# Optimization experiments

Measured on AMD Instinct MI355X. Metric: run time of the kernel, lower is better.

Reference implementation:

```python
import jax, jax.numpy as jnp
import numpy as np

B, S, D, H = 2, 4096, 512, 8
DK = D // H


def setup_inputs() -> dict:
    key = jax.random.key(0)
    ks = jax.random.split(key, 8)
    q = jax.random.normal(ks[0], (B, S, D), dtype=jnp.float32)
    k = jax.random.normal(ks[1], (B, S, D), dtype=jnp.float32)
    v = jax.random.normal(ks[2], (B, S, D), dtype=jnp.float32)
    mask = jax.random.randint(ks[3], (B, S, S), 0, 2, dtype=jnp.int32)
    scale = 1.0 / np.sqrt(D)
    w_q = jax.random.normal(ks[4], (D, D), dtype=jnp.float32) * scale
    w_k = jax.random.normal(ks[5], (D, D), dtype=jnp.float32) * scale
    w_v = jax.random.normal(ks[6], (D, D), dtype=jnp.float32) * scale
    w_o = jax.random.normal(ks[7], (D, D), dtype=jnp.float32) * scale
    return {"q": q, "k": k, "v": v, "mask": mask,
            "w_q": w_q, "w_k": w_k, "w_v": w_v, "w_o": w_o}


def reference(q, k, v, mask, w_q, w_k, w_v, w_o):
    # Projections (weights stored as [in, out]; no bias, matching bias=False)
    # [B,S,D] -> [B,H,S,DK]
    def split_heads(x):
        return x.reshape(B, S, H, DK).transpose(0, 2, 1, 3)

    qh = split_heads(q @ w_q)
    kh = split_heads(k @ w_k)
    vh = split_heads(v @ w_v)

    inv_sqrt_dk = jnp.float32(1.0 / np.sqrt(DK))
    # Explicit O(S^2) score matrix, as in the original module
    scores = jnp.einsum('bhqd,bhkd->bhqk', qh, kh) * inv_sqrt_dk
    scores = jnp.where(mask[:, None, :, :] == 0, jnp.float32(-1e9), scores)
    attn = jax.nn.softmax(scores, axis=-1)
    # dropout in eval mode (p=0) -> identity
    x = jnp.einsum('bhqk,bhkd->bhqd', attn, vh)
    x = x.transpose(0, 2, 1, 3).reshape(B, S, D)
    return x @ w_o
```

## Files before the change

### kernel.cpp

```cpp
#include <hip/hip_runtime.h>
#include <hip/hip_bf16.h>

#define Bn 2
#define Sn 4096
#define Dn 512
#define Hn 8
#define DKn 64

typedef __attribute__((ext_vector_type(8))) short bf16x8;
typedef __attribute__((ext_vector_type(4))) float f32x4;
typedef __attribute__((ext_vector_type(4))) _Float16 f16x4;
typedef __attribute__((ext_vector_type(8))) _Float16 f16x8;
typedef __attribute__((ext_vector_type(2))) _Float16 f16x2;
typedef __attribute__((ext_vector_type(8))) unsigned short us8;
typedef __attribute__((ext_vector_type(4))) unsigned short us4;

__device__ __forceinline__ unsigned short f2bf(float f) {
  unsigned u = __builtin_bit_cast(unsigned, f);
  u += 0x7fffu + ((u >> 16) & 1u);
  return (unsigned short)(u >> 16);
}

__global__ __launch_bounds__(256) void pack_mask_k(const int* __restrict__ mask,
                                                   unsigned int* __restrict__ pm) {
  int gid = blockIdx.x * 256 + threadIdx.x;
  int m = mask[gid];
  unsigned long long bal = __ballot(m != 0);
  if ((threadIdx.x & 63) == 0) {
    int q = (gid >> 12) & 4095;
    int b = gid >> 24;
    int kvw = (gid >> 5) & 127;
    pm[((size_t)b * 128 + kvw) * 4096 + q] = (unsigned)bal;
    pm[((size_t)b * 128 + kvw + 1) * 4096 + q] = (unsigned)(bal >> 32);
  }
}

__global__ __launch_bounds__(256) void cvt_k(const float* __restrict__ q,
                                             const float* __restrict__ k,
                                             const float* __restrict__ v,
                                             unsigned short* __restrict__ o) {
  const float* src = blockIdx.y == 0 ? q : blockIdx.y == 1 ? k : v;
  size_t i = (size_t)blockIdx.x * 256 + threadIdx.x;
  float4 f = *(const float4*)&src[i * 4];
  us4 r = {f2bf(f.x), f2bf(f.y), f2bf(f.z), f2bf(f.w)};
  *(us4*)&o[(size_t)blockIdx.y * (Bn * Sn * Dn) + i * 4] = r;
}

__global__ __launch_bounds__(256) void wt_k(const float* __restrict__ wq,
                                            const float* __restrict__ wk,
                                            const float* __restrict__ wv,
                                            const float* __restrict__ wo,
                                            unsigned short* __restrict__ wt) {
  __shared__ unsigned short ls[64][68];
  const float* W = blockIdx.z == 0 ? wq : blockIdx.z == 1 ? wk
                 : blockIdx.z == 2 ? wv : wo;
  int k0 = blockIdx.x * 64, n0 = blockIdx.y * 64;
  int t = threadIdx.x;
  for (int j = 0; j < 4; ++j) {
    int i = t + j * 256;
    int r = i >> 4, c4 = (i & 15) << 2;
    float4 f = *(const float4*)&W[(size_t)(k0 + r) * 512 + n0 + c4];
    ls[c4 + 0][r] = f2bf(f.x);
    ls[c4 + 1][r] = f2bf(f.y);
    ls[c4 + 2][r] = f2bf(f.z);
    ls[c4 + 3][r] = f2bf(f.w);
  }
  __syncthreads();
  unsigned short* out = wt + (size_t)blockIdx.z * 512 * 512;
  for (int j = 0; j < 4; ++j) {
    int i = t + j * 256;
    int r = i >> 4, c4 = (i & 15) << 2;
    us4 v = {ls[r][c4], ls[r][c4 + 1], ls[r][c4 + 2], ls[r][c4 + 3]};
    *(us4*)&out[(size_t)(n0 + r) * 512 + k0 + c4] = v;
  }
}

template <int MT, bool HEADS>
__global__ __launch_bounds__(256, 2) void gemm_k(
    const unsigned short* __restrict__ A0, size_t zstride,
    const unsigned short* __restrict__ wt, unsigned short* __restrict__ oh,
    unsigned short* __restrict__ vtg, float* __restrict__ olin) {
  __shared__ unsigned short smem[MT * 8192 + 16384];
  const int z = blockIdx.z;
  const unsigned short* A = A0 + zstride * z;
  const unsigned short* Wt = wt + (size_t)z * 512 * 512;
  const float scale = (HEADS && z == 0) ? 0.125f * 1.44269504088896f : 1.0f;
  const int m0 = blockIdx.x * (MT * 64), n0 = blockIdx.y * 128;
  const int t = threadIdx.x, w = t >> 6, l = t & 63;
  const int quad = l >> 4, c = l & 15;

  f32x4 acc[MT][8] = {};
  us8 apre[MT * 2], bpre[4];

#pragma unroll
  for (int j = 0; j < MT * 2; ++j) {
    int i = t + j * 256, r = i >> 3, u = i & 7;
    apre[j] = *(const us8*)&A[(size_t)(m0 + r) * 512 + (u << 3)];
  }
#pragma unroll
  for (int j = 0; j < 4; ++j) {
    int i = t + j * 256, r = i >> 3, u = i & 7;
    bpre[j] = *(const us8*)&Wt[(size_t)(n0 + r) * 512 + (u << 3)];
  }
#pragma unroll
  for (int j = 0; j < MT * 2; ++j) {
    int i = t + j * 256, r = i >> 3, u = i & 7;
    *(us8*)&smem[r * 64 + ((u ^ (r & 7)) << 3)] = apre[j];
  }
#pragma unroll
  for (int j = 0; j < 4; ++j) {
    int i = t + j * 256, r = i >> 3, u = i & 7;
    *(us8*)&smem[MT * 8192 + r * 64 + ((u ^ (r & 7)) << 3)] = bpre[j];
  }

  for (int k0 = 0; k0 < 512; k0 += 64) {
    const int cur = (k0 >> 6) & 1;
    const unsigned short* AsC = &smem[cur * (MT * 4096)];
    const unsigned short* BsC = &smem[MT * 8192 + cur * 8192];
    __syncthreads();
    const bool nxt = k0 + 64 < 512;
    if (nxt) {
#pragma unroll
      for (int j = 0; j < MT * 2; ++j) {
        int i = t + j * 256, r = i >> 3, u = i & 7;
        apre[j] = *(const us8*)&A[(size_t)(m0 + r) * 512 + k0 + 64 + (u << 3)];
      }
#pragma unroll
      for (int j = 0; j < 4; ++j) {
        int i = t + j * 256, r = i >> 3, u = i & 7;
        bpre[j] = *(const us8*)&Wt[(size_t)(n0 + r) * 512 + k0 + 64 + (u << 3)];
      }
    }

#pragma unroll
    for (int kc = 0; kc < 2; ++kc) {
      bf16x8 aA[MT], bB[8];
      int u = kc * 4 + quad;
#pragma unroll
      for (int mt = 0; mt < MT; ++mt) {
        int row = w * (MT * 16) + mt * 16 + c;
        aA[mt] = *(const bf16x8*)&AsC[row * 64 + ((u ^ (c & 7)) << 3)];
      }
#pragma unroll
      for (int nt = 0; nt < 8; ++nt) {
        int row = nt * 16 + c;
        bB[nt] = *(const bf16x8*)&BsC[row * 64 + ((u ^ (c & 7)) << 3)];
      }
#pragma unroll
      for (int mt = 0; mt < MT; ++mt)
#pragma unroll
        for (int nt = 0; nt < 8; ++nt)
          acc[mt][nt] = __builtin_amdgcn_mfma_f32_16x16x32_bf16(
              aA[mt], bB[nt], acc[mt][nt], 0, 0, 0);
    }

    if (nxt) {
      unsigned short* AsN = &smem[(cur ^ 1) * (MT * 4096)];
      unsigned short* BsN = &smem[MT * 8192 + (cur ^ 1) * 8192];
#pragma unroll
      for (int j = 0; j < MT * 2; ++j) {
        int i = t + j * 256, r = i >> 3, u = i & 7;
        *(us8*)&AsN[r * 64 + ((u ^ (r & 7)) << 3)] = apre[j];
      }
#pragma unroll
      for (int j = 0; j < 4; ++j) {
        int i = t + j * 256, r = i >> 3, u = i & 7;
        *(us8*)&BsN[r * 64 + ((u ^ (r & 7)) << 3)] = bpre[j];
      }
    }
  }

  if constexpr (HEADS) {
    if (z == 2) {
      __syncthreads();
#pragma unroll
      for (int mt = 0; mt < MT; ++mt) {
        int mb = w * (MT * 16) + mt * 16 + (quad << 2);
        int ml = (mb & 64) | (((mb >> 5) & 1) << 5) | (((mb >> 2) & 3) << 3) |
                 (((mb >> 4) & 1) << 2);
#pragma unroll
        for (int nt = 0; nt < 8; ++nt) {
          int nl = nt * 16 + c;
          us4 pk;
#pragma unroll
          for (int r = 0; r < 4; ++r)
            pk[r] = __builtin_bit_cast(unsigned short, (_Float16)acc[mt][nt][r]);
          *(us4*)&smem[nl * 152 + ml] = pk;
        }
      }
      __syncthreads();
      const int bb = m0 >> 12, sb = m0 & 4095;
#pragma unroll
      for (int j = 0; j < MT * 4; ++j) {
        int i = t + j * 256;
        int nl = i >> 4, mc = (i & 15) << 3;
        us8 vv = *(const us8*)&smem[nl * 152 + mc];
        int n = n0 + nl, hh = n >> 6, dk = n & 63;
        *(us8*)&vtg[((size_t)(bb * Hn + hh) * DKn + dk) * Sn + sb + mc] = vv;
      }
    } else {
#pragma unroll
      for (int mt = 0; mt < MT; ++mt)
#pragma unroll
        for (int nt = 0; nt < 8; ++nt)
#pragma unroll
          for (int r = 0; r < 4; ++r) {
            int m = m0 + w * (MT * 16) + mt * 16 + (quad << 2) + r;
            int n = n0 + nt * 16 + c;
            int b = m >> 12, s = m & 4095, hh = n >> 6, dk = n & 63;
            oh[(size_t)z * (Bn * Hn * Sn * DKn) +
               ((size_t)(b * Hn + hh) * Sn + s) * DKn + dk] =
                f2bf(acc[mt][nt][r] * scale);
          }
    }
  } else {
#pragma unroll
    for (int mt = 0; mt < MT; ++mt)
#pragma unroll
      for (int nt = 0; nt < 8; ++nt)
#pragma unroll
        for (int r = 0; r < 4; ++r) {
          int m = m0 + w * (MT * 16) + mt * 16 + (quad << 2) + r;
          int n = n0 + nt * 16 + c;
          olin[(size_t)m * 512 + n] = acc[mt][nt][r];
        }
  }
}

__global__ __launch_bounds__(512, 4) void flash_k(
    const unsigned short* __restrict__ Qh, const unsigned short* __restrict__ Kh,
    const unsigned short* __restrict__ VtG, const unsigned int* __restrict__ pmt,
    unsigned short* __restrict__ attn) {
  __shared__ unsigned short Ks[2][2][64 * 64];
  __shared__ unsigned short Vts[2][2][64 * 64];
  __shared__ unsigned int Mw[2][2][256];

  const int q0 = blockIdx.x * 128, h = blockIdx.y, b = blockIdx.z;
  const int t = threadIdx.x;
  const int g = t >> 8, tg = t & 255;
  const int w = (t >> 6) & 3, l = t & 63;
  const int quad = l >> 4, c = l & 15;
  const size_t hb = (size_t)(b * Hn + h) * Sn * DKn;
  const unsigned short* Qg = Qh + hb;
  const unsigned short* Kg = Kh + hb;
  const unsigned short* Vg = VtG + hb;

  bf16x8 bQ[2][2];
#pragma unroll
  for (int qf = 0; qf < 2; ++qf) {
    int qrow = q0 + w * 32 + qf * 16 + c;
#pragma unroll
    for (int kc = 0; kc < 2; ++kc)
      bQ[qf][kc] = *(const bf16x8*)&Qg[(size_t)qrow * 64 + kc * 32 + quad * 8];
  }

  f32x4 oacc[2][4] = {};
  float lsum[2] = {};
  const int sr = tg >> 3, su = tg & 7;
  const int off0 = sr * 64 + ((su ^ (sr & 7)) << 3);
  const int off1 = (sr + 32) * 64 + ((su ^ (sr & 7)) << 3);
  const f16x2 one2 = {(_Float16)1.0f, (_Float16)1.0f};

  us8 kpre[2], vpre[2];
  unsigned mpre;
  {
    const int kvF = g * 64;
    kpre[0] = *(const us8*)&Kg[(size_t)(kvF + sr) * 64 + (su << 3)];
    kpre[1] = *(const us8*)&Kg[(size_t)(kvF + sr + 32) * 64 + (su << 3)];
    vpre[0] = *(const us8*)&Vg[(size_t)sr * Sn + kvF + (su << 3)];
    vpre[1] = *(const us8*)&Vg[(size_t)(sr + 32) * Sn + kvF + (su << 3)];
    mpre = pmt[((size_t)b * 128 + (kvF >> 5) + (tg >> 7)) * 4096 + q0 + (tg & 127)];
    *(us8*)&Ks[g][0][off0] = kpre[0];
    *(us8*)&Ks[g][0][off1] = kpre[1];
    *(us8*)&Vts[g][0][off0] = vpre[0];
    *(us8*)&Vts[g][0][off1] = vpre[1];
    Mw[g][0][tg] = mpre;
  }

  for (int it = 0; it < 32; ++it) {
    const int cur = it & 1;
    __syncthreads();
    const bool nxt = it + 1 < 32;
    if (nxt) {
      const int kvN = (2 * (it + 1) + g) * 64;
      kpre[0] = *(const us8*)&Kg[(size_t)(kvN + sr) * 64 + (su << 3)];
      kpre[1] = *(const us8*)&Kg[(size_t)(kvN + sr + 32) * 64 + (su << 3)];
      vpre[0] = *(const us8*)&Vg[(size_t)sr * Sn + kvN + (su << 3)];
      vpre[1] = *(const us8*)&Vg[(size_t)(sr + 32) * Sn + kvN + (su << 3)];
      mpre = pmt[((size_t)b * 128 + (kvN >> 5) + (tg >> 7)) * 4096 + q0 + (tg & 127)];
    }

    f32x4 sacc[2][4] = {};
#pragma unroll
    for (int kc = 0; kc < 2; ++kc) {
      int u = kc * 4 + quad;
#pragma unroll
      for (int kvt = 0; kvt < 4; ++kvt) {
        int row = kvt * 16 + c;
        bf16x8 aK = *(const bf16x8*)&Ks[g][cur][row * 64 + ((u ^ (c & 7)) << 3)];
#pragma unroll
        for (int qf = 0; qf < 2; ++qf)
          sacc[qf][kvt] = __builtin_amdgcn_mfma_f32_16x16x32_bf16(
              aK, bQ[qf][kc], sacc[qf][kvt], 0, 0, 0);
      }
    }

    f16x8 ph[2][2];
#pragma unroll
    for (int qf = 0; qf < 2; ++qf) {
      int qloc = w * 32 + qf * 16 + c;
      unsigned mv0 = Mw[g][cur][qloc], mv1 = Mw[g][cur][128 + qloc];
#pragma unroll
      for (int half = 0; half < 2; ++half) {
        unsigned word = half ? mv1 : mv0;
        uint4 ww;
#pragma unroll
        for (int kvh = 0; kvh < 2; ++kvh) {
          unsigned bits = (word >> ((kvh << 4) + (quad << 2))) & 15u;
          const f32x4 s4 = sacc[qf][half * 2 + kvh];
          float p0 = (bits & 1u) ? __builtin_amdgcn_exp2f(s4[0]) : 0.f;
          float p1 = (bits & 2u) ? __builtin_amdgcn_exp2f(s4[1]) : 0.f;
          float p2 = (bits & 4u) ? __builtin_amdgcn_exp2f(s4[2]) : 0.f;
          float p3 = (bits & 8u) ? __builtin_amdgcn_exp2f(s4[3]) : 0.f;
          f16x2 a = __builtin_bit_cast(f16x2, __builtin_amdgcn_cvt_pkrtz(p0, p1));
          f16x2 bpk = __builtin_bit_cast(f16x2, __builtin_amdgcn_cvt_pkrtz(p2, p3));
          lsum[qf] = __builtin_amdgcn_fdot2(a, one2, lsum[qf], false);
          lsum[qf] = __builtin_amdgcn_fdot2(bpk, one2, lsum[qf], false);
          (&ww.x)[kvh * 2] = __builtin_bit_cast(unsigned, a);
          (&ww.x)[kvh * 2 + 1] = __builtin_bit_cast(unsigned, bpk);
        }
        ph[qf][half] = __builtin_bit_cast(f16x8, ww);
      }
    }

#pragma unroll
    for (int half = 0; half < 2; ++half) {
      int u2 = half * 4 + quad;
#pragma unroll
      for (int dkt = 0; dkt < 4; ++dkt) {
        int dk = dkt * 16 + c;
        f16x8 bV = __builtin_bit_cast(
            f16x8, *(const us8*)&Vts[g][cur][dk * 64 + ((u2 ^ (c & 7)) << 3)]);
#pragma unroll
        for (int qf = 0; qf < 2; ++qf)
          oacc[qf][dkt] = __builtin_amdgcn_mfma_f32_16x16x32_f16(
              ph[qf][half], bV, oacc[qf][dkt], 0, 0, 0);
      }
    }

    if (nxt) {
      const int nb = cur ^ 1;
      *(us8*)&Ks[g][nb][off0] = kpre[0];
      *(us8*)&Ks[g][nb][off1] = kpre[1];
      *(us8*)&Vts[g][nb][off0] = vpre[0];
      *(us8*)&Vts[g][nb][off1] = vpre[1];
      Mw[g][nb][tg] = mpre;
    }
  }

  __syncthreads();
  float* fsum = (float*)&Ks[0][0][0];
  float* flsum = (float*)&Vts[0][0][0];
  if (g == 1) {
#pragma unroll
    for (int qf = 0; qf < 2; ++qf) {
#pragma unroll
      for (int dkt = 0; dkt < 4; ++dkt)
        *(f32x4*)&fsum[(((qf * 4 + dkt) * 4 + w) * 64 + l) * 4] = oacc[qf][dkt];
      flsum[(qf * 4 + w) * 64 + l] = lsum[qf];
    }
  }
  __syncthreads();
  if (g == 0) {
#pragma unroll
    for (int qf = 0; qf < 2; ++qf) {
      lsum[qf] += flsum[(qf * 4 + w) * 64 + l];
#pragma unroll
      for (int dkt = 0; dkt < 4; ++dkt) {
        f32x4 o1 = *(const f32x4*)&fsum[(((qf * 4 + dkt) * 4 + w) * 64 + l) * 4];
#pragma unroll
        for (int r = 0; r < 4; ++r) oacc[qf][dkt][r] += o1[r];
      }
    }
#pragma unroll
    for (int qf = 0; qf < 2; ++qf) {
      float s = lsum[qf];
      s += __shfl_xor(s, 16, 64);
      s += __shfl_xor(s, 32, 64);
      float inv = 1.0f / s;
#pragma unroll
      for (int r = 0; r < 4; ++r) {
        float invr = __shfl(inv, (quad << 2) + r, 64);
        unsigned short* dst =
            &attn[((size_t)(b * Sn + q0 + w * 32 + qf * 16 + (quad << 2) + r)) * Dn +
                  h * 64 + c];
#pragma unroll
        for (int dkt = 0; dkt < 4; ++dkt)
          dst[dkt * 16] = f2bf(oacc[qf][dkt][r] * invr);
      }
    }
  }
}

extern "C" void kernel_launch(void* const* d_in, const int* in_sizes, int n_in,
                              void* d_out, int out_size, void* d_ws,
                              size_t ws_size, hipStream_t stream) {
  const float* q = (const float*)d_in[0];
  const float* k = (const float*)d_in[1];
  const float* v = (const float*)d_in[2];
  const int* mask = (const int*)d_in[3];
  const float* wq = (const float*)d_in[4];
  const float* wk = (const float*)d_in[5];
  const float* wv = (const float*)d_in[6];
  const float* wo = (const float*)d_in[7];
  float* out = (float*)d_out;

  char* ws = (char*)d_ws;
  const size_t headN = (size_t)Bn * Hn * Sn * DKn;
  const size_t tensB = headN * 2;
  unsigned short* qbkb = (unsigned short*)ws;
  unsigned short* attn = (unsigned short*)ws;
  size_t off = 3 * tensB;
  unsigned short* qkv = (unsigned short*)(ws + off);
  off += 3 * tensB;
  unsigned short* wt = (unsigned short*)(ws + off);
  off += 4ull * 512 * 512 * 2;
  unsigned int* pm = (unsigned int*)(ws + off);

  pack_mask_k<<<(Bn * Sn * Sn) / 256, 256, 0, stream>>>(mask, pm);
  cvt_k<<<dim3(4096, 3), 256, 0, stream>>>(q, k, v, qbkb);
  wt_k<<<dim3(8, 8, 4), 256, 0, stream>>>(wq, wk, wv, wo, wt);
  gemm_k<2, true><<<dim3(64, 4, 3), 256, 0, stream>>>(
      qbkb, headN, wt, qkv, qkv + 2 * headN, nullptr);
  flash_k<<<dim3(32, 8, 2), 512, 0, stream>>>(qkv, qkv + headN,
                                              qkv + 2 * headN, pm, attn);
  gemm_k<1, false><<<dim3(128, 4, 1), 256, 0, stream>>>(
      attn, 0, wt + 3ull * 512 * 512, nullptr, nullptr, out);
}
```

Baseline: 388.2 us.

## Fuse prep kernels, convert fp32 inputs inside GEMM, compute row sums via MFMA

The mask packing and weight transpose kernels are merged into one prep kernel, and the mask-packing blocks now loop over eight chunks each. The separate fp32-to-bf16 conversion of q/k/v is dropped; the projection GEMM reads fp32 directly and converts while loading tiles. This removes a full write and re-read of the converted activations plus two launches. In the flash kernel, the softmax row sums move from fdot2 accumulation onto an extra MFMA against a ones vector, which also removes the end-of-kernel shuffles. Pointer increments replace per-iteration address recomputation. In exchange, the GEMM pulls twice as many bytes from global memory per A tile, and each flash iteration issues more MFMAs.

```diff
diff --git a/kernel.cpp b/kernel.cpp
--- a/kernel.cpp
+++ b/kernel.cpp
@@ -21,68 +21,60 @@
   return (unsigned short)(u >> 16);
 }
 
-__global__ __launch_bounds__(256) void pack_mask_k(const int* __restrict__ mask,
-                                                   unsigned int* __restrict__ pm) {
-  int gid = blockIdx.x * 256 + threadIdx.x;
-  int m = mask[gid];
-  unsigned long long bal = __ballot(m != 0);
-  if ((threadIdx.x & 63) == 0) {
-    int q = (gid >> 12) & 4095;
-    int b = gid >> 24;
-    int kvw = (gid >> 5) & 127;
-    pm[((size_t)b * 128 + kvw) * 4096 + q] = (unsigned)bal;
-    pm[((size_t)b * 128 + kvw + 1) * 4096 + q] = (unsigned)(bal >> 32);
-  }
-}
-
-__global__ __launch_bounds__(256) void cvt_k(const float* __restrict__ q,
-                                             const float* __restrict__ k,
-                                             const float* __restrict__ v,
-                                             unsigned short* __restrict__ o) {
-  const float* src = blockIdx.y == 0 ? q : blockIdx.y == 1 ? k : v;
-  size_t i = (size_t)blockIdx.x * 256 + threadIdx.x;
-  float4 f = *(const float4*)&src[i * 4];
-  us4 r = {f2bf(f.x), f2bf(f.y), f2bf(f.z), f2bf(f.w)};
-  *(us4*)&o[(size_t)blockIdx.y * (Bn * Sn * Dn) + i * 4] = r;
-}
-
-__global__ __launch_bounds__(256) void wt_k(const float* __restrict__ wq,
-                                            const float* __restrict__ wk,
-                                            const float* __restrict__ wv,
-                                            const float* __restrict__ wo,
-                                            unsigned short* __restrict__ wt) {
-  __shared__ unsigned short ls[64][68];
-  const float* W = blockIdx.z == 0 ? wq : blockIdx.z == 1 ? wk
-                 : blockIdx.z == 2 ? wv : wo;
-  int k0 = blockIdx.x * 64, n0 = blockIdx.y * 64;
-  int t = threadIdx.x;
-  for (int j = 0; j < 4; ++j) {
-    int i = t + j * 256;
-    int r = i >> 4, c4 = (i & 15) << 2;
-    float4 f = *(const float4*)&W[(size_t)(k0 + r) * 512 + n0 + c4];
-    ls[c4 + 0][r] = f2bf(f.x);
-    ls[c4 + 1][r] = f2bf(f.y);
-    ls[c4 + 2][r] = f2bf(f.z);
-    ls[c4 + 3][r] = f2bf(f.w);
-  }
-  __syncthreads();
-  unsigned short* out = wt + (size_t)blockIdx.z * 512 * 512;
-  for (int j = 0; j < 4; ++j) {
-    int i = t + j * 256;
-    int r = i >> 4, c4 = (i & 15) << 2;
-    us4 v = {ls[r][c4], ls[r][c4 + 1], ls[r][c4 + 2], ls[r][c4 + 3]};
-    *(us4*)&out[(size_t)(n0 + r) * 512 + k0 + c4] = v;
+__global__ __launch_bounds__(256) void prep_k(
+    const int* __restrict__ mask, unsigned int* __restrict__ pm,
+    const float* __restrict__ wq, const float* __restrict__ wk,
+    const float* __restrict__ wv, const float* __restrict__ wo,
+    unsigned short* __restrict__ wt) {
+  const int t = threadIdx.x;
+  if (blockIdx.x < 256) {
+    __shared__ unsigned short ls[64][68];
+    int bid = blockIdx.x;
+    int z = bid >> 6, x = bid & 7, y = (bid >> 3) & 7;
+    const float* W = z == 0 ? wq : z == 1 ? wk : z == 2 ? wv : wo;
+    int k0 = x * 64, n0 = y * 64;
+    for (int j = 0; j < 4; ++j) {
+      int i = t + j * 256;
+      int r = i >> 4, c4 = (i & 15) << 2;
+      float4 f = *(const float4*)&W[(size_t)(k0 + r) * 512 + n0 + c4];
+      ls[c4 + 0][r] = f2bf(f.x);
+      ls[c4 + 1][r] = f2bf(f.y);
+      ls[c4 + 2][r] = f2bf(f.z);
+      ls[c4 + 3][r] = f2bf(f.w);
+    }
+    __syncthreads();
+    unsigned short* out = wt + (size_t)z * 512 * 512;
+    for (int j = 0; j < 4; ++j) {
+      int i = t + j * 256;
+      int r = i >> 4, c4 = (i & 15) << 2;
+      us4 v = {ls[r][c4], ls[r][c4 + 1], ls[r][c4 + 2], ls[r][c4 + 3]};
+      *(us4*)&out[(size_t)(n0 + r) * 512 + k0 + c4] = v;
+    }
+  } else {
+    size_t idx = (size_t)(blockIdx.x - 256) * 256 + t;
+    for (int it = 0; it < 8; ++it, idx += 4194304) {
+      int m = mask[idx];
+      unsigned long long bal = __ballot(m != 0);
+      if ((t & 63) == 0) {
+        int q = (int)((idx >> 12) & 4095);
+        int b = (int)(idx >> 24);
+        int kvw = (int)((idx >> 5) & 127);
+        pm[((size_t)b * 128 + kvw) * 4096 + q] = (unsigned)bal;
+        pm[((size_t)b * 128 + kvw + 1) * 4096 + q] = (unsigned)(bal >> 32);
+      }
+    }
   }
 }
 
 template <int MT, bool HEADS>
 __global__ __launch_bounds__(256, 2) void gemm_k(
-    const unsigned short* __restrict__ A0, size_t zstride,
+    const float* __restrict__ aq, const float* __restrict__ ak,
+    const float* __restrict__ av, const unsigned short* __restrict__ abf,
     const unsigned short* __restrict__ wt, unsigned short* __restrict__ oh,
     unsigned short* __restrict__ vtg, float* __restrict__ olin) {
   __shared__ unsigned short smem[MT * 8192 + 16384];
   const int z = blockIdx.z;
-  const unsigned short* A = A0 + zstride * z;
+  const float* A32 = HEADS ? (z == 0 ? aq : z == 1 ? ak : av) : nullptr;
   const unsigned short* Wt = wt + (size_t)z * 512 * 512;
   const float scale = (HEADS && z == 0) ? 0.125f * 1.44269504088896f : 1.0f;
   const int m0 = blockIdx.x * (MT * 64), n0 = blockIdx.y * 128;
@@ -92,11 +84,23 @@
   f32x4 acc[MT][8] = {};
   us8 apre[MT * 2], bpre[4];
 
-#pragma unroll
-  for (int j = 0; j < MT * 2; ++j) {
+  auto ldA = [&](int j, int kk) -> us8 {
     int i = t + j * 256, r = i >> 3, u = i & 7;
-    apre[j] = *(const us8*)&A[(size_t)(m0 + r) * 512 + (u << 3)];
-  }
+    if constexpr (HEADS) {
+      const float* s = &A32[(size_t)(m0 + r) * 512 + kk + (u << 3)];
+      float4 f0 = *(const float4*)s;
+      float4 f1 = *(const float4*)(s + 4);
+      us8 v;
+      v[0] = f2bf(f0.x); v[1] = f2bf(f0.y); v[2] = f2bf(f0.z); v[3] = f2bf(f0.w);
+      v[4] = f2bf(f1.x); v[5] = f2bf(f1.y); v[6] = f2bf(f1.z); v[7] = f2bf(f1.w);
+      return v;
+    } else {
+      return *(const us8*)&abf[(size_t)(m0 + r) * 512 + kk + (u << 3)];
+    }
+  };
+
+#pragma unroll
+  for (int j = 0; j < MT * 2; ++j) apre[j] = ldA(j, 0);
 #pragma unroll
   for (int j = 0; j < 4; ++j) {
     int i = t + j * 256, r = i >> 3, u = i & 7;
@@ -121,10 +125,7 @@
     const bool nxt = k0 + 64 < 512;
     if (nxt) {
 #pragma unroll
-      for (int j = 0; j < MT * 2; ++j) {
-        int i = t + j * 256, r = i >> 3, u = i & 7;
-        apre[j] = *(const us8*)&A[(size_t)(m0 + r) * 512 + k0 + 64 + (u << 3)];
-      }
+      for (int j = 0; j < MT * 2; ++j) apre[j] = ldA(j, k0 + 64);
 #pragma unroll
       for (int j = 0; j < 4; ++j) {
         int i = t + j * 256, r = i >> 3, u = i & 7;
@@ -242,8 +243,6 @@
   const int quad = l >> 4, c = l & 15;
   const size_t hb = (size_t)(b * Hn + h) * Sn * DKn;
   const unsigned short* Qg = Qh + hb;
-  const unsigned short* Kg = Kh + hb;
-  const unsigned short* Vg = VtG + hb;
 
   bf16x8 bQ[2][2];
 #pragma unroll
@@ -255,39 +254,46 @@
   }
 
   f32x4 oacc[2][4] = {};
-  float lsum[2] = {};
+  f32x4 oaccl[2] = {};
+  f16x8 vone8;
+#pragma unroll
+  for (int i = 0; i < 8; ++i) vone8[i] = (_Float16)1.0f;
+
   const int sr = tg >> 3, su = tg & 7;
   const int off0 = sr * 64 + ((su ^ (sr & 7)) << 3);
   const int off1 = (sr + 32) * 64 + ((su ^ (sr & 7)) << 3);
-  const f16x2 one2 = {(_Float16)1.0f, (_Float16)1.0f};
+
+  const unsigned short* kp0 = Kh + hb + ((size_t)(g * 64 + sr)) * 64 + (su << 3);
+  const unsigned short* kp1 = kp0 + 32 * 64;
+  const unsigned short* vp0 = VtG + hb + (size_t)sr * Sn + g * 64 + (su << 3);
+  const unsigned short* vp1 = VtG + hb + (size_t)(sr + 32) * Sn + g * 64 + (su << 3);
+  const unsigned int* mp =
+      pmt + ((size_t)b * 128 + g * 2 + (tg >> 7)) * 4096 + q0 + (tg & 127);
 
   us8 kpre[2], vpre[2];
   unsigned mpre;
-  {
-    const int kvF = g * 64;
-    kpre[0] = *(const us8*)&Kg[(size_t)(kvF + sr) * 64 + (su << 3)];
-    kpre[1] = *(const us8*)&Kg[(size_t)(kvF + sr + 32) * 64 + (su << 3)];
-    vpre[0] = *(const us8*)&Vg[(size_t)sr * Sn + kvF + (su << 3)];
-    vpre[1] = *(const us8*)&Vg[(size_t)(sr + 32) * Sn + kvF + (su << 3)];
-    mpre = pmt[((size_t)b * 128 + (kvF >> 5) + (tg >> 7)) * 4096 + q0 + (tg & 127)];
-    *(us8*)&Ks[g][0][off0] = kpre[0];
-    *(us8*)&Ks[g][0][off1] = kpre[1];
-    *(us8*)&Vts[g][0][off0] = vpre[0];
-    *(us8*)&Vts[g][0][off1] = vpre[1];
-    Mw[g][0][tg] = mpre;
-  }
+  kpre[0] = *(const us8*)kp0;
+  kpre[1] = *(const us8*)kp1;
+  vpre[0] = *(const us8*)vp0;
+  vpre[1] = *(const us8*)vp1;
+  mpre = *mp;
+  *(us8*)&Ks[g][0][off0] = kpre[0];
+  *(us8*)&Ks[g][0][off1] = kpre[1];
+  *(us8*)&Vts[g][0][off0] = vpre[0];
+  *(us8*)&Vts[g][0][off1] = vpre[1];
+  Mw[g][0][tg] = mpre;
 
   for (int it = 0; it < 32; ++it) {
     const int cur = it & 1;
     __syncthreads();
     const bool nxt = it + 1 < 32;
     if (nxt) {
-      const int kvN = (2 * (it + 1) + g) * 64;
-      kpre[0] = *(const us8*)&Kg[(size_t)(kvN + sr) * 64 + (su << 3)];
-      kpre[1] = *(const us8*)&Kg[(size_t)(kvN + sr + 32) * 64 + (su << 3)];
-      vpre[0] = *(const us8*)&Vg[(size_t)sr * Sn + kvN + (su << 3)];
-      vpre[1] = *(const us8*)&Vg[(size_t)(sr + 32) * Sn + kvN + (su << 3)];
-      mpre = pmt[((size_t)b * 128 + (kvN >> 5) + (tg >> 7)) * 4096 + q0 + (tg & 127)];
+      kp0 += 8192; kp1 += 8192; vp0 += 128; vp1 += 128; mp += 16384;
+      kpre[0] = *(const us8*)kp0;
+      kpre[1] = *(const us8*)kp1;
+      vpre[0] = *(const us8*)vp0;
+      vpre[1] = *(const us8*)vp1;
+      mpre = *mp;
     }
 
     f32x4 sacc[2][4] = {};
@@ -324,8 +330,6 @@
           float p3 = (bits & 8u) ? __builtin_amdgcn_exp2f(s4[3]) : 0.f;
           f16x2 a = __builtin_bit_cast(f16x2, __builtin_amdgcn_cvt_pkrtz(p0, p1));
           f16x2 bpk = __builtin_bit_cast(f16x2, __builtin_amdgcn_cvt_pkrtz(p2, p3));
-          lsum[qf] = __builtin_amdgcn_fdot2(a, one2, lsum[qf], false);
-          lsum[qf] = __builtin_amdgcn_fdot2(bpk, one2, lsum[qf], false);
           (&ww.x)[kvh * 2] = __builtin_bit_cast(unsigned, a);
           (&ww.x)[kvh * 2 + 1] = __builtin_bit_cast(unsigned, bpk);
         }
@@ -346,6 +350,10 @@
           oacc[qf][dkt] = __builtin_amdgcn_mfma_f32_16x16x32_f16(
               ph[qf][half], bV, oacc[qf][dkt], 0, 0, 0);
       }
+#pragma unroll
+      for (int qf = 0; qf < 2; ++qf)
+        oaccl[qf] = __builtin_amdgcn_mfma_f32_16x16x32_f16(
+            ph[qf][half], vone8, oaccl[qf], 0, 0, 0);
     }
 
     if (nxt) {
@@ -367,14 +375,16 @@
 #pragma unroll
       for (int dkt = 0; dkt < 4; ++dkt)
         *(f32x4*)&fsum[(((qf * 4 + dkt) * 4 + w) * 64 + l) * 4] = oacc[qf][dkt];
-      flsum[(qf * 4 + w) * 64 + l] = lsum[qf];
+      *(f32x4*)&flsum[((qf * 4 + w) * 64 + l) * 4] = oaccl[qf];
     }
   }
   __syncthreads();
   if (g == 0) {
 #pragma unroll
     for (int qf = 0; qf < 2; ++qf) {
-      lsum[qf] += flsum[(qf * 4 + w) * 64 + l];
+      f32x4 l1 = *(const f32x4*)&flsum[((qf * 4 + w) * 64 + l) * 4];
+#pragma unroll
+      for (int r = 0; r < 4; ++r) oaccl[qf][r] += l1[r];
 #pragma unroll
       for (int dkt = 0; dkt < 4; ++dkt) {
         f32x4 o1 = *(const f32x4*)&fsum[(((qf * 4 + dkt) * 4 + w) * 64 + l) * 4];
@@ -383,14 +393,10 @@
       }
     }
 #pragma unroll
-    for (int qf = 0; qf < 2; ++qf) {
-      float s = lsum[qf];
-      s += __shfl_xor(s, 16, 64);
-      s += __shfl_xor(s, 32, 64);
-      float inv = 1.0f / s;
+    for (int qf = 0; qf < 2; ++qf)
 #pragma unroll
       for (int r = 0; r < 4; ++r) {
-        float invr = __shfl(inv, (quad << 2) + r, 64);
+        float invr = 1.0f / oaccl[qf][r];
         unsigned short* dst =
             &attn[((size_t)(b * Sn + q0 + w * 32 + qf * 16 + (quad << 2) + r)) * Dn +
                   h * 64 + c];
@@ -398,7 +404,6 @@
         for (int dkt = 0; dkt < 4; ++dkt)
           dst[dkt * 16] = f2bf(oacc[qf][dkt][r] * invr);
       }
-    }
   }
 }
 
@@ -418,7 +423,6 @@
   char* ws = (char*)d_ws;
   const size_t headN = (size_t)Bn * Hn * Sn * DKn;
   const size_t tensB = headN * 2;
-  unsigned short* qbkb = (unsigned short*)ws;
   unsigned short* attn = (unsigned short*)ws;
   size_t off = 3 * tensB;
   unsigned short* qkv = (unsigned short*)(ws + off);
@@ -427,13 +431,12 @@
   off += 4ull * 512 * 512 * 2;
   unsigned int* pm = (unsigned int*)(ws + off);
 
-  pack_mask_k<<<(Bn * Sn * Sn) / 256, 256, 0, stream>>>(mask, pm);
-  cvt_k<<<dim3(4096, 3), 256, 0, stream>>>(q, k, v, qbkb);
-  wt_k<<<dim3(8, 8, 4), 256, 0, stream>>>(wq, wk, wv, wo, wt);
+  prep_k<<<16640, 256, 0, stream>>>(mask, pm, wq, wk, wv, wo, wt);
   gemm_k<2, true><<<dim3(64, 4, 3), 256, 0, stream>>>(
-      qbkb, headN, wt, qkv, qkv + 2 * headN, nullptr);
+      q, k, v, nullptr, wt, qkv, qkv + 2 * headN, nullptr);
   flash_k<<<dim3(32, 8, 2), 512, 0, stream>>>(qkv, qkv + headN,
                                               qkv + 2 * headN, pm, attn);
   gemm_k<1, false><<<dim3(128, 4, 1), 256, 0, stream>>>(
-      attn, 0, wt + 3ull * 512 * 512, nullptr, nullptr, out);
+      nullptr, nullptr, nullptr, attn, wt + 3ull * 512 * 512, nullptr, nullptr,
+      out);
 }
```

After: 366.4 us. -5.6%, faster.
